# Kernel tuning notes

Measured on AMD Instinct MI355X. Metric: run time of the kernel, lower is better.

Reference implementation:

```python
import jax, jax.numpy as jnp
import numpy as np

C = 80           # foreground classes
B, N = 8, 4000   # images, proposals per image
K_PRE = 2048     # pre-NMS candidates per image (fixed-shape stand-in for torch.where filtering)
DET = 100        # detection_per_image
SCORE_THRESH = 0.01
NMS_THRESH = 0.5
MIN_AREA = 0.1
BBOX_W = (10.0, 10.0, 5.0, 5.0)
CLIP = float(np.log(1000.0 / 16.0))
CLS_OFFSET = 4096.0               # > max image coordinate, for batched (per-class) NMS


def setup_inputs() -> dict:
    key = jax.random.key(0)
    k1, k2, k3, k4 = jax.random.split(key, 4)
    p1 = jax.random.uniform(k1, (B, N, 2)) * 800.0
    wh = jax.random.uniform(k2, (B, N, 2)) * 200.0 + 1.0
    proposals = jnp.concatenate([p1, p1 + wh], axis=-1)          # [B,N,4] x1,y1,x2,y2
    label_pre = jax.random.normal(k3, (B, N, C + 1), dtype=jnp.float32)
    bbox_pre = jax.random.normal(k4, (B, N, (C + 1) * 4), dtype=jnp.float32) * 0.5
    return {"label_pre": label_pre, "bbox_pre": bbox_pre, "proposals": proposals}


def decode_boxes(deltas, props):
    w = props[..., 2] - props[..., 0]
    h = props[..., 3] - props[..., 1]
    cx = props[..., 0] + 0.5 * w
    cy = props[..., 1] + 0.5 * h
    dx = deltas[..., 0] / BBOX_W[0]
    dy = deltas[..., 1] / BBOX_W[1]
    dw = jnp.minimum(deltas[..., 2] / BBOX_W[2], CLIP)
    dh = jnp.minimum(deltas[..., 3] / BBOX_W[3], CLIP)
    pcx = dx * w + cx
    pcy = dy * h + cy
    pw = jnp.exp(dw) * w
    ph = jnp.exp(dh) * h
    return jnp.stack([pcx - 0.5 * pw, pcy - 0.5 * ph,
                      pcx + 0.5 * pw, pcy + 0.5 * ph], axis=-1)


def pairwise_iou(b):
    # b [K,4] -> [K,K]
    area = jnp.maximum(b[:, 2] - b[:, 0], 0.0) * jnp.maximum(b[:, 3] - b[:, 1], 0.0)
    lt = jnp.maximum(b[:, None, :2], b[None, :, :2])
    rb = jnp.minimum(b[:, None, 2:], b[None, :, 2:])
    wh = jnp.maximum(rb - lt, 0.0)
    inter = wh[..., 0] * wh[..., 1]
    union = area[:, None] + area[None, :] - inter
    return inter / jnp.maximum(union, 1e-9)


def greedy_nms_keep(boxes, valid):
    # boxes already sorted by score (descending); returns kept mask
    K = boxes.shape[0]
    iou = pairwise_iou(boxes)
    idx = jnp.arange(K)

    def body(i, keep):
        sup = (iou[i] > NMS_THRESH) & (idx > i) & keep[i]
        return keep & ~sup

    return jax.lax.fori_loop(0, K, body, valid)


def process_image(logits, deltas, props):
    probs = jax.nn.softmax(logits, axis=-1)            # [N, C+1]
    scores = probs[:, 1:].reshape(-1)                  # [N*C]
    d = deltas[:, 4:].reshape(N, C, 4)                 # drop background deltas
    boxes = decode_boxes(d, props[:, None, :]).reshape(-1, 4)   # [N*C, 4]
    labels = jnp.broadcast_to(jnp.arange(1, C + 1), (N, C)).reshape(-1)
    area = (boxes[:, 3] - boxes[:, 1]) * (boxes[:, 2] - boxes[:, 0])
    valid = (scores > SCORE_THRESH) & (area > MIN_AREA)
    masked = jnp.where(valid, scores, -1.0)
    top_scores, top_idx = jax.lax.top_k(masked, K_PRE)
    top_boxes = boxes[top_idx]
    top_labels = labels[top_idx]
    keep0 = top_scores > 0.0
    # batched_nms: per-class coordinate offset so classes never suppress each other
    off = (top_labels.astype(top_boxes.dtype) * CLS_OFFSET)[:, None]
    keep = greedy_nms_keep(top_boxes + off, keep0)
    final = jnp.where(keep, top_scores, -1.0)
    det_scores, det_idx = jax.lax.top_k(final, DET)
    return top_boxes[det_idx], det_scores, top_labels[det_idx]


def reference(label_pre, bbox_pre, proposals):
    # returns (boxes [B,DET,4], scores [B,DET], labels [B,DET]); entries with score<0 are padding
    return jax.vmap(process_image)(label_pre, bbox_pre, proposals)
```

## Files before the change

### kernel.cpp

```cpp
#include <hip/hip_runtime.h>
#include <stdint.h>

#define B_ 8
#define N_ 4000
#define C_ 80
#define NC_ (N_ * C_)
#define KP_ 2048
#define CAND_ 4096
#define SLOTS_ 32
#define SLOTCAP_ 128
#define DET_ 100
#define NW_ 32
#define CLIP_ 4.135166556742356f

#define PB_ 16
#define IB_ (N_ / PB_)
#define CB_ 64
#define SEGB_ 64
#define U4PT_ 5

#define RT_ 256
#define RI_ 4
#define RJS_ 16
#define RSL_ (CAND_ / RJS_)
#define RIB_ (CAND_ / (RT_ * RI_))
#define IBK_ (CAND_ / 256)

typedef unsigned long long u64;

__device__ __forceinline__ void decode4(const float4 pr, const float4 d,
                                        float& x1, float& y1, float& x2, float& y2) {
  float w = pr.z - pr.x, h = pr.w - pr.y;
  float cx = pr.x + 0.5f * w, cy = pr.y + 0.5f * h;
  float dx = d.x / 10.0f, dy = d.y / 10.0f;
  float dw = fminf(d.z / 5.0f, CLIP_), dh = fminf(d.w / 5.0f, CLIP_);
  float pcx = dx * w + cx, pcy = dy * h + cy;
  float pw = expf(dw) * w, ph = expf(dh) * h;
  x1 = pcx - 0.5f * pw; y1 = pcy - 0.5f * ph;
  x2 = pcx + 0.5f * pw; y2 = pcy + 0.5f * ph;
}

__device__ __forceinline__ uint32_t coarse_sum(const uint32_t* __restrict__ histPart,
                                               int b, int t, uint32_t (*wsum)[CB_]) {
  int l = t & 63, wv = t >> 6;
  uint32_t v = 0;
  for (int j = wv; j < IB_; j += 4)
    v += histPart[((size_t)b * IB_ + j) * CB_ + l];
  wsum[wv][l] = v;
  __syncthreads();
  return (t < CB_) ? (wsum[0][t] + wsum[1][t] + wsum[2][t] + wsum[3][t]) : 0u;
}

__global__ __launch_bounds__(256) void k_scores(const float* __restrict__ logits,
                                                uint32_t* __restrict__ keys,
                                                uint32_t* __restrict__ histPart,
                                                uint4* __restrict__ zr, int zrN) {
  __shared__ float lds[PB_ * 81];
  __shared__ float mArr[PB_], dArr[PB_];
  __shared__ uint32_t hcnt[CB_];
  int blk = blockIdx.x;
  int b = blk / IB_, lb = blk - b * IB_;
  int p0 = b * N_ + lb * PB_;
  int t = threadIdx.x;
  for (int i = blk * 256 + t; i < zrN; i += B_ * IB_ * 256)
    zr[i] = make_uint4(0u, 0u, 0u, 0u);
  if (t < CB_) hcnt[t] = 0;
  const float4* src = (const float4*)(logits + (size_t)p0 * 81);
  for (int k = t; k < PB_ * 81 / 4; k += 256) ((float4*)lds)[k] = src[k];
  __syncthreads();
  if (t < PB_) {
    const float* lp = lds + t * 81;
    float m = lp[0];
    for (int i = 1; i <= C_; ++i) m = fmaxf(m, lp[i]);
    float denom = 0.f;
    for (int i = 0; i <= C_; ++i) denom += expf(lp[i] - m);
    mArr[t] = m; dArr[t] = denom;
  }
  __syncthreads();
#pragma unroll
  for (int iter = 0; iter < PB_ * C_ / 256; ++iter) {
    int e = iter * 256 + t;
    int pp = e / C_, c = e - pp * C_;
    float lv = lds[pp * 81 + c + 1];
    float score = expf(lv - mArr[pp]) / dArr[pp];
    uint32_t key = 0;
    if (score > 0.01f) {
      key = __float_as_uint(score);
      atomicAdd(&hcnt[(key >> 20) - 960], 1u);
    }
    keys[(size_t)p0 * C_ + e] = key;
  }
  __syncthreads();
  if (t < CB_) histPart[((size_t)b * IB_ + lb) * CB_ + t] = hcnt[t];
}

__global__ __launch_bounds__(256) void k_compact(const uint32_t* __restrict__ keys,
                                                 const uint32_t* __restrict__ histPart,
                                                 uint32_t* __restrict__ cnt,
                                                 u64* __restrict__ cand) {
  __shared__ uint32_t wsum[4][CB_];
  __shared__ uint32_t s_thr;
  int blk = blockIdx.x;
  int b = blk / SEGB_, lb = blk - b * SEGB_;
  int t = threadIdx.x;
  uint32_t cv = coarse_sum(histPart, b, t, wsum);
  if (t < CB_) {
    uint32_t v = cv;
#pragma unroll
    for (int d = 1; d < 64; d <<= 1) {
      uint32_t o = __shfl_down(v, d);
      v += (t + d < 64) ? o : 0;
    }
    uint32_t nxt = __shfl_down(v, 1);
    if (t == 63) nxt = 0;
    uint32_t total = __shfl(v, 0);
    if (t == 0 && total < KP_) s_thr = 1u;
    if (total >= KP_ && v >= KP_ && nxt < KP_)
      s_thr = ((uint32_t)(t + 960)) << 20;
  }
  __syncthreads();
  uint32_t thrb = s_thr;
  const uint4* kp4 = (const uint4*)(keys + (size_t)b * NC_);
#pragma unroll
  for (int q = 0; q < U4PT_; ++q) {
    int ti = lb * (256 * U4PT_) + q * 256 + t;
    if (ti >= NC_ / 4) break;
    uint4 k4 = kp4[ti];
    int slot = (ti >> 4) & (SLOTS_ - 1);
    uint32_t kv[4] = {k4.x, k4.y, k4.z, k4.w};
    int ns = 0;
#pragma unroll
    for (int qq = 0; qq < 4; ++qq) ns += (kv[qq] >= thrb) ? 1 : 0;
    if (ns == 0) continue;
    uint32_t pos = atomicAdd(&cnt[(b * SLOTS_ + slot) * 16], (uint32_t)ns);
    u64* seg = cand + (size_t)b * CAND_ + slot * SLOTCAP_;
    uint32_t baseIdx = (uint32_t)(ti * 4);
#pragma unroll
    for (int qq = 0; qq < 4; ++qq) {
      if (kv[qq] >= thrb) {
        if (pos < SLOTCAP_)
          seg[pos] = ((u64)kv[qq] << 32) | (uint32_t)(~(baseIdx + qq));
        ++pos;
      }
    }
  }
}

__global__ __launch_bounds__(256) void k_rank(const u64* __restrict__ cand,
                                              uint32_t* __restrict__ rankPart) {
  __shared__ u64 sh[RSL_];
  int blk = blockIdx.x;
  int b = blk / (RIB_ * RJS_);
  int rem = blk - b * (RIB_ * RJS_);
  int lb = rem / RJS_, js = rem - lb * RJS_;
  int t = threadIdx.x;
  const u64* cb2 = cand + (size_t)b * CAND_;
  if (t < RSL_ / 2)
    ((ulonglong2*)sh)[t] = ((const ulonglong2*)(cb2 + js * RSL_))[t];
  int base = lb * (RT_ * RI_) + t;
  u64 ki[RI_];
#pragma unroll
  for (int q = 0; q < RI_; ++q) ki[q] = cb2[base + q * RT_];
  __syncthreads();
  int cnt4[RI_] = {0, 0, 0, 0};
#pragma unroll 4
  for (int j2 = 0; j2 < RSL_ / 2; ++j2) {
    ulonglong2 v = ((const ulonglong2*)sh)[j2];
#pragma unroll
    for (int q = 0; q < RI_; ++q) {
      cnt4[q] += (v.x > ki[q]) ? 1 : 0;
      cnt4[q] += (v.y > ki[q]) ? 1 : 0;
    }
  }
  uint32_t* rp = rankPart + ((size_t)(b * RJS_ + js)) * CAND_ + base;
#pragma unroll
  for (int q = 0; q < RI_; ++q) rp[q * RT_] = (uint32_t)cnt4[q];
}

__global__ __launch_bounds__(256) void k_scatter(
    const u64* __restrict__ cand, const uint32_t* __restrict__ rankPart,
    const float* __restrict__ bbox, const float* __restrict__ props,
    float* __restrict__ topScore, int* __restrict__ topLabel,
    float* __restrict__ topBox, float* __restrict__ nmsBox) {
  int blk = blockIdx.x;
  int b = blk / IBK_, lb = blk - b * IBK_;
  int t = threadIdx.x;
  int i = lb * 256 + t;
  u64 ki = cand[(size_t)b * CAND_ + i];
  if (ki == 0ull) return;
  uint32_t r = 0;
#pragma unroll
  for (int js = 0; js < RJS_; ++js)
    r += rankPart[((size_t)(b * RJS_ + js)) * CAND_ + i];
  if (r >= KP_) return;
  uint32_t sbits = (uint32_t)(ki >> 32);
  uint32_t idx = ~((uint32_t)ki);
  int n = idx / C_, c = idx % C_;
  float4 pr4 = ((const float4*)props)[(size_t)b * N_ + n];
  float4 d = ((const float4*)(bbox + ((size_t)b * N_ + n) * ((C_ + 1) * 4)))[c + 1];
  float x1, y1, x2, y2;
  decode4(pr4, d, x1, y1, x2, y2);
  float off = (float)(c + 1) * 4096.0f;
  size_t o = (size_t)b * KP_ + (size_t)r;
  topScore[o] = __uint_as_float(sbits);
  topLabel[o] = c + 1;
  ((float4*)topBox)[o] = make_float4(x1, y1, x2, y2);
  ((float4*)nmsBox)[o] = make_float4(x1 + off, y1 + off, x2 + off, y2 + off);
}

__global__ __launch_bounds__(64) void k_supmat(const float* __restrict__ nmsBox,
                                               u64* __restrict__ sup) {
  int blk = blockIdx.x;
  int b = blk / 528, r = blk - b * 528;
  int ti = 0, rem = r;
  while (rem >= 32 - ti) { rem -= 32 - ti; ++ti; }
  int tj = ti + rem;
  __shared__ float4 shj[64];
  __shared__ float sha[64];
  int l = threadIdx.x;
  const float4* boxes = (const float4*)(nmsBox + (size_t)b * KP_ * 4);
  float4 bj0 = boxes[tj * 64 + l];
  shj[l] = bj0;
  sha[l] = fmaxf(bj0.z - bj0.x, 0.f) * fmaxf(bj0.w - bj0.y, 0.f);
  int i = ti * 64 + l;
  float4 bi = boxes[i];
  float areai = fmaxf(bi.z - bi.x, 0.f) * fmaxf(bi.w - bi.y, 0.f);
  __syncthreads();
  u64 bits = 0;
  for (int jj = 0; jj < 64; ++jj) {
    int j = tj * 64 + jj;
    if (j > i) {
      float4 bj = shj[jj];
      float ltx = fmaxf(bi.x, bj.x), lty = fmaxf(bi.y, bj.y);
      float rbx = fminf(bi.z, bj.z), rby = fminf(bi.w, bj.w);
      float iw = fmaxf(rbx - ltx, 0.f), ih = fmaxf(rby - lty, 0.f);
      float inter = iw * ih;
      float uni = areai + sha[jj] - inter;
      float iou = inter / fmaxf(uni, 1e-9f);
      if (iou > 0.5f) bits |= (1ull << jj);
    }
  }
  sup[((size_t)b * KP_ + i) * NW_ + tj] = bits;
}

__global__ __launch_bounds__(64) void k_nms_scan(const u64* __restrict__ sup,
                                                 const float* __restrict__ topScore,
                                                 const int* __restrict__ topLabel,
                                                 const float* __restrict__ topBox,
                                                 float* __restrict__ out) {
  int b = blockIdx.x, l = threadIdx.x;
  int h = l >> 5, w = l & 31;
  const u64* base = sup + (size_t)b * KP_ * NW_;
  const float* ts = topScore + (size_t)b * KP_;
  const int* tl = topLabel + (size_t)b * KP_;
  const float4* tb = (const float4*)(topBox + (size_t)b * KP_ * 4);
  unsigned m32 = 0;
#pragma unroll
  for (int j = 0; j < 8; ++j) {
    float4 s4 = ((const float4*)ts)[l * 8 + j];
    if (!(s4.x > 0.f)) m32 |= 1u << (4 * j + 0);
    if (!(s4.y > 0.f)) m32 |= 1u << (4 * j + 1);
    if (!(s4.z > 0.f)) m32 |= 1u << (4 * j + 2);
    if (!(s4.w > 0.f)) m32 |= 1u << (4 * j + 3);
  }
  u64 removed = ((u64)__shfl(m32, 2 * w + 1) << 32) | (u64)__shfl(m32, 2 * w);

  int outCount = 0;
  auto emitRow = [&](int row, bool kept) {
    if (l == (outCount & 63)) {
      float4 bx = tb[row];
      out[((size_t)b * DET_ + outCount) * 4 + 0] = bx.x;
      out[((size_t)b * DET_ + outCount) * 4 + 1] = bx.y;
      out[((size_t)b * DET_ + outCount) * 4 + 2] = bx.z;
      out[((size_t)b * DET_ + outCount) * 4 + 3] = bx.w;
      out[B_ * DET_ * 4 + (size_t)b * DET_ + outCount] = kept ? ts[row] : -1.0f;
      out[B_ * DET_ * 4 + B_ * DET_ + (size_t)b * DET_ + outCount] = (float)tl[row];
    }
    ++outCount;
  };

  u64 ra[32], rb[32];
  auto loadc = [&](u64* dst, int c) {
    const u64* p = base + ((size_t)c * 64 + h * 32) * NW_ + w;
#pragma unroll
    for (int k = 0; k < 32; ++k) dst[k] = p[(size_t)k * NW_];
  };
  auto chunk = [&](u64* cur, int c) -> bool {
    u64 rm = __shfl(removed, c);
    unsigned rml = (unsigned)rm, rmh = (unsigned)(rm >> 32);
#pragma unroll
    for (int k = 0; k < 32; ++k) {
      unsigned dlo = __builtin_amdgcn_readlane((unsigned)cur[k], c);
      unsigned dhi = __builtin_amdgcn_readlane((unsigned)(cur[k] >> 32), c);
      if (!((rml >> k) & 1u)) { rml |= dlo; rmh |= dhi; }
    }
#pragma unroll
    for (int k = 0; k < 32; ++k) {
      unsigned dlo = __builtin_amdgcn_readlane((unsigned)cur[k], 32 + c);
      unsigned dhi = __builtin_amdgcn_readlane((unsigned)(cur[k] >> 32), 32 + c);
      if (!((rmh >> k) & 1u)) { rml |= dlo; rmh |= dhi; }
    }
    u64 rmfull = ((u64)rmh << 32) | rml;
    u64 kb = ~rmfull;
    while (kb) {
      if (outCount >= DET_) return true;
      int k = __builtin_ctzll(kb);
      kb &= kb - 1;
      emitRow(c * 64 + k, true);
    }
    if (outCount >= DET_) return true;
    unsigned kmask = h ? ~rmh : ~rml;
    u64 acc = 0;
#pragma unroll
    for (int k = 0; k < 32; ++k)
      acc |= ((kmask >> k) & 1u) ? cur[k] : 0ull;
    acc |= __shfl_xor(acc, 32);
    removed = (l == c) ? rmfull : removed;
    if (l < 32 && l >= c) removed |= acc;
    return false;
  };

  bool done = false;
  loadc(ra, 0);
  for (int c = 0; c < NW_ && !done; c += 2) {
    if (c + 1 < NW_) loadc(rb, c + 1);
    done = chunk(ra, c);
    if (!done) {
      if (c + 2 < NW_) loadc(ra, c + 2);
      done = chunk(rb, c + 1);
    }
  }
  if (outCount < DET_) {
    for (int c2 = 0; c2 < NW_ && outCount < DET_; ++c2) {
      u64 rm = __shfl(removed, c2);
      while (rm && outCount < DET_) {
        int k = __builtin_ctzll(rm);
        rm &= rm - 1;
        emitRow(c2 * 64 + k, false);
      }
    }
  }
}

extern "C" void kernel_launch(void* const* d_in, const int* in_sizes, int n_in,
                              void* d_out, int out_size, void* d_ws, size_t ws_size,
                              hipStream_t stream) {
  const float* label_pre = (const float*)d_in[0];
  const float* bbox_pre = (const float*)d_in[1];
  const float* props = (const float*)d_in[2];
  float* out = (float*)d_out;

  char* ws = (char*)d_ws;
  size_t off = 0;
  auto alloc = [&](size_t bytes) -> void* {
    void* p = ws + off;
    off = (off + bytes + 255) & ~(size_t)255;
    return p;
  };

  uint32_t* keys = (uint32_t*)alloc((size_t)B_ * NC_ * 4);
  uint32_t* histPart = (uint32_t*)alloc((size_t)B_ * IB_ * CB_ * 4);
  size_t zero_begin = off;
  uint32_t* cnt = (uint32_t*)alloc((size_t)B_ * SLOTS_ * 16 * 4);
  u64* cand = (u64*)alloc((size_t)B_ * CAND_ * 8);
  float* topScore = (float*)alloc((size_t)B_ * KP_ * 4);
  int* topLabel = (int*)alloc((size_t)B_ * KP_ * 4);
  float* topBox = (float*)alloc((size_t)B_ * KP_ * 16);
  float* nmsBox = (float*)alloc((size_t)B_ * KP_ * 16);
  size_t zero_end = off;
  u64* sup = (u64*)alloc((size_t)B_ * KP_ * NW_ * 8);
  uint32_t* rankPart = (uint32_t*)alloc((size_t)B_ * RJS_ * CAND_ * 4);

  if (off > ws_size) return;

  uint4* zr = (uint4*)(ws + zero_begin);
  int zrN = (int)((zero_end - zero_begin) / 16);

  k_scores<<<B_ * IB_, 256, 0, stream>>>(label_pre, keys, histPart, zr, zrN);
  k_compact<<<B_ * SEGB_, 256, 0, stream>>>(keys, histPart, cnt, cand);
  k_rank<<<B_ * RIB_ * RJS_, RT_, 0, stream>>>(cand, rankPart);
  k_scatter<<<B_ * IBK_, 256, 0, stream>>>(cand, rankPart, bbox_pre, props,
                                           topScore, topLabel, topBox, nmsBox);
  k_supmat<<<B_ * 528, 64, 0, stream>>>(nmsBox, sup);
  k_nms_scan<<<B_, 64, 0, stream>>>(sup, topScore, topLabel, topBox, out);
}
```

Baseline: 186.2 us.

## Fuse suppression-matrix build and NMS scan into one per-image lazy kernel

Replaces the separate IoU bitmask kernel and the serial scan kernel with one 1024-thread block per image. Each 64-row chunk of the suppression matrix is computed into shared memory just before the scan consumes it, and the loop exits once 100 detections are emitted. This removes the global round trip of the full bitmask matrix and skips IoU rows that are never needed. In exchange, only 8 blocks run, so IoU throughput across the GPU is much lower. Each chunk also pays two block barriers while one wavefront scans and the rest sit idle. Separately, the per-block proposal count in the score kernel goes from 16 to 80.

```diff
diff --git a/kernel.cpp b/kernel.cpp
--- a/kernel.cpp
+++ b/kernel.cpp
@@ -13,7 +13,7 @@
 #define NW_ 32
 #define CLIP_ 4.135166556742356f
 
-#define PB_ 16
+#define PB_ 80
 #define IB_ (N_ / PB_)
 #define CB_ 64
 #define SEGB_ 64
@@ -208,64 +208,44 @@
   ((float4*)nmsBox)[o] = make_float4(x1 + off, y1 + off, x2 + off, y2 + off);
 }
 
-__global__ __launch_bounds__(64) void k_supmat(const float* __restrict__ nmsBox,
-                                               u64* __restrict__ sup) {
-  int blk = blockIdx.x;
-  int b = blk / 528, r = blk - b * 528;
-  int ti = 0, rem = r;
-  while (rem >= 32 - ti) { rem -= 32 - ti; ++ti; }
-  int tj = ti + rem;
-  __shared__ float4 shj[64];
-  __shared__ float sha[64];
-  int l = threadIdx.x;
-  const float4* boxes = (const float4*)(nmsBox + (size_t)b * KP_ * 4);
-  float4 bj0 = boxes[tj * 64 + l];
-  shj[l] = bj0;
-  sha[l] = fmaxf(bj0.z - bj0.x, 0.f) * fmaxf(bj0.w - bj0.y, 0.f);
-  int i = ti * 64 + l;
-  float4 bi = boxes[i];
-  float areai = fmaxf(bi.z - bi.x, 0.f) * fmaxf(bi.w - bi.y, 0.f);
-  __syncthreads();
-  u64 bits = 0;
-  for (int jj = 0; jj < 64; ++jj) {
-    int j = tj * 64 + jj;
-    if (j > i) {
-      float4 bj = shj[jj];
-      float ltx = fmaxf(bi.x, bj.x), lty = fmaxf(bi.y, bj.y);
-      float rbx = fminf(bi.z, bj.z), rby = fminf(bi.w, bj.w);
-      float iw = fmaxf(rbx - ltx, 0.f), ih = fmaxf(rby - lty, 0.f);
-      float inter = iw * ih;
-      float uni = areai + sha[jj] - inter;
-      float iou = inter / fmaxf(uni, 1e-9f);
-      if (iou > 0.5f) bits |= (1ull << jj);
-    }
-  }
-  sup[((size_t)b * KP_ + i) * NW_ + tj] = bits;
-}
-
-__global__ __launch_bounds__(64) void k_nms_scan(const u64* __restrict__ sup,
-                                                 const float* __restrict__ topScore,
-                                                 const int* __restrict__ topLabel,
-                                                 const float* __restrict__ topBox,
-                                                 float* __restrict__ out) {
-  int b = blockIdx.x, l = threadIdx.x;
-  int h = l >> 5, w = l & 31;
-  const u64* base = sup + (size_t)b * KP_ * NW_;
+__global__ __launch_bounds__(1024) void k_nms_fused(
+    const float* __restrict__ topScore, const int* __restrict__ topLabel,
+    const float* __restrict__ topBox, const float* __restrict__ nmsBox,
+    float* __restrict__ out) {
+  __shared__ float4 sbox[KP_];
+  __shared__ float sarea[KP_];
+  __shared__ u64 srow[64][NW_];
+  __shared__ int s_done;
+  int b = blockIdx.x, t = threadIdx.x;
+  const float4* nb = (const float4*)(nmsBox + (size_t)b * KP_ * 4);
+  for (int i = t; i < KP_; i += 1024) {
+    float4 bx = nb[i];
+    sbox[i] = bx;
+    sarea[i] = fmaxf(bx.z - bx.x, 0.f) * fmaxf(bx.w - bx.y, 0.f);
+  }
+  if (t == 0) s_done = 0;
+
   const float* ts = topScore + (size_t)b * KP_;
   const int* tl = topLabel + (size_t)b * KP_;
   const float4* tb = (const float4*)(topBox + (size_t)b * KP_ * 4);
-  unsigned m32 = 0;
-#pragma unroll
-  for (int j = 0; j < 8; ++j) {
-    float4 s4 = ((const float4*)ts)[l * 8 + j];
-    if (!(s4.x > 0.f)) m32 |= 1u << (4 * j + 0);
-    if (!(s4.y > 0.f)) m32 |= 1u << (4 * j + 1);
-    if (!(s4.z > 0.f)) m32 |= 1u << (4 * j + 2);
-    if (!(s4.w > 0.f)) m32 |= 1u << (4 * j + 3);
-  }
-  u64 removed = ((u64)__shfl(m32, 2 * w + 1) << 32) | (u64)__shfl(m32, 2 * w);
-
+
+  int l = t & 63, h = l >> 5, w = l & 31;
+  u64 removed = 0;
   int outCount = 0;
+  if (t < 64) {
+    unsigned m32 = 0;
+#pragma unroll
+    for (int j = 0; j < 8; ++j) {
+      float4 s4 = ((const float4*)ts)[l * 8 + j];
+      if (!(s4.x > 0.f)) m32 |= 1u << (4 * j + 0);
+      if (!(s4.y > 0.f)) m32 |= 1u << (4 * j + 1);
+      if (!(s4.z > 0.f)) m32 |= 1u << (4 * j + 2);
+      if (!(s4.w > 0.f)) m32 |= 1u << (4 * j + 3);
+    }
+    removed = ((u64)__shfl(m32, 2 * w + 1) << 32) | (u64)__shfl(m32, 2 * w);
+  }
+  __syncthreads();
+
   auto emitRow = [&](int row, bool kept) {
     if (l == (outCount & 63)) {
       float4 bx = tb[row];
@@ -279,13 +259,10 @@
     ++outCount;
   };
 
-  u64 ra[32], rb[32];
-  auto loadc = [&](u64* dst, int c) {
-    const u64* p = base + ((size_t)c * 64 + h * 32) * NW_ + w;
-#pragma unroll
-    for (int k = 0; k < 32; ++k) dst[k] = p[(size_t)k * NW_];
-  };
-  auto chunk = [&](u64* cur, int c) -> bool {
+  auto scanChunk = [&](int c) -> bool {
+    u64 cur[NW_];
+#pragma unroll
+    for (int k = 0; k < 32; ++k) cur[k] = srow[h * 32 + k][w];
     u64 rm = __shfl(removed, c);
     unsigned rml = (unsigned)rm, rmh = (unsigned)(rm >> 32);
 #pragma unroll
@@ -320,17 +297,44 @@
     return false;
   };
 
-  bool done = false;
-  loadc(ra, 0);
-  for (int c = 0; c < NW_ && !done; c += 2) {
-    if (c + 1 < NW_) loadc(rb, c + 1);
-    done = chunk(ra, c);
-    if (!done) {
-      if (c + 2 < NW_) loadc(ra, c + 2);
-      done = chunk(rb, c + 1);
-    }
-  }
-  if (outCount < DET_) {
+  int r = t >> 4;
+  int w0 = (t & 15) << 1;
+  for (int c = 0; c < NW_; ++c) {
+    {
+      int i = c * 64 + r;
+      float4 bi = sbox[i];
+      float ai = sarea[i];
+#pragma unroll
+      for (int ww = 0; ww < 2; ++ww) {
+        int wd = w0 + ww;
+        u64 bits = 0;
+        for (int jj = 0; jj < 64; ++jj) {
+          int j = wd * 64 + jj;
+          if (j > i) {
+            float4 bj = sbox[j];
+            float ltx = fmaxf(bi.x, bj.x), lty = fmaxf(bi.y, bj.y);
+            float rbx = fminf(bi.z, bj.z), rby = fminf(bi.w, bj.w);
+            float iw = fmaxf(rbx - ltx, 0.f), ih = fmaxf(rby - lty, 0.f);
+            float inter = iw * ih;
+            float uni = ai + sarea[j] - inter;
+            float iou = inter / fmaxf(uni, 1e-9f);
+            if (iou > 0.5f) bits |= (1ull << jj);
+          }
+        }
+        srow[r][wd] = bits;
+      }
+    }
+    __syncthreads();
+    if (t < 64) {
+      if (scanChunk(c)) {
+        if (l == 0) s_done = 1;
+      }
+    }
+    __syncthreads();
+    if (s_done) break;
+  }
+
+  if (t < 64 && outCount < DET_) {
     for (int c2 = 0; c2 < NW_ && outCount < DET_; ++c2) {
       u64 rm = __shfl(removed, c2);
       while (rm && outCount < DET_) {
@@ -368,7 +372,6 @@
   float* topBox = (float*)alloc((size_t)B_ * KP_ * 16);
   float* nmsBox = (float*)alloc((size_t)B_ * KP_ * 16);
   size_t zero_end = off;
-  u64* sup = (u64*)alloc((size_t)B_ * KP_ * NW_ * 8);
   uint32_t* rankPart = (uint32_t*)alloc((size_t)B_ * RJS_ * CAND_ * 4);
 
   if (off > ws_size) return;
@@ -381,6 +384,5 @@
   k_rank<<<B_ * RIB_ * RJS_, RT_, 0, stream>>>(cand, rankPart);
   k_scatter<<<B_ * IBK_, 256, 0, stream>>>(cand, rankPart, bbox_pre, props,
                                            topScore, topLabel, topBox, nmsBox);
-  k_supmat<<<B_ * 528, 64, 0, stream>>>(nmsBox, sup);
-  k_nms_scan<<<B_, 64, 0, stream>>>(sup, topScore, topLabel, topBox, out);
-}
+  k_nms_fused<<<B_, 1024, 0, stream>>>(topScore, topLabel, topBox, nmsBox, out);
+}
```

New measurement: 327.4 us. 1.76x slower.
